# Kernel tuning notes

Hardware: AMD Instinct MI355X
Metric: run time of the kernel (lower is better)

Reference implementation:

```python
import jax, jax.numpy as jnp
import numpy as np

# Matches init_kwargs: zip(dilation_rates, sequence_lengths)
DILATION_RATES = (1, 2, 4)
SEQUENCE_LENGTHS = (2048, 4096, 8192)


def setup_inputs() -> dict:
    key = jax.random.key(0)
    qkv = jax.random.normal(key, (4, 8192, 3, 16, 64), dtype=jnp.float32)
    return {"qkv": qkv}


def _attend(x, scale):
    # x: (B', Nseg, 3, h, d) -- vanilla softmax attention over axis Nseg
    q, k, v = x[:, :, 0], x[:, :, 1], x[:, :, 2]
    scores = jnp.einsum('bnhd,bmhd->bhnm', q, k) * scale
    attn = jax.nn.softmax(scores, axis=-1)
    return jnp.einsum('bhnm,bmhd->bnhd', attn, v)  # (B', Nseg, h, d)


def reference(qkv):
    b, n, _, h, d = qkv.shape
    scale = 1.0 / jnp.sqrt(jnp.asarray(d, qkv.dtype))  # softmax_scale=None default
    out = jnp.zeros((b, n, h, d), qkv.dtype)
    for r, s in zip(DILATION_RATES, SEQUENCE_LENGTHS):
        nseg = n // s
        # 'b (n s) qkv h d -> b n s qkv h d' then dilated slice [::r]
        x = qkv.reshape(b, nseg, s, 3, h, d)[:, :, ::r]  # (b, nseg, sp, 3, h, d)
        sp = x.shape[2]
        # 'b n s qkv h d -> (b s) n qkv h d'
        x = x.transpose(0, 2, 1, 3, 4, 5).reshape(b * sp, nseg, 3, h, d)
        o = _attend(x, scale)  # (b*sp, nseg, h, d)
        # '(b s) n h d -> b n s h d'
        o = o.reshape(b, sp, nseg, h, d).transpose(0, 2, 1, 3, 4)
        # strided scatter-add back into the full-length accumulator
        out = out.reshape(b, nseg, s, h, d).at[:, :, ::r].add(o).reshape(b, n, h, d)
    # final global normalization over the sequence dim (as in the source)
    return out / out.sum(axis=1, keepdims=True)
```

## Files before the change

### kernel.cpp

```cpp
#include <hip/hip_runtime.h>

constexpr int   Bn    = 4;
constexpr int   Nn    = 8192;
constexpr int   Hn    = 16;
constexpr int   Dn    = 64;
constexpr int   ROW   = 3 * Hn * Dn;
constexpr long long QKV_B = (long long)Nn * ROW;
constexpr int   OUT_N = Hn * Dn;
constexpr long long OUT_B = (long long)Nn * OUT_N;

template<int CTRL>
__device__ __forceinline__ float dpp_add(float x) {
  int mv = __builtin_amdgcn_update_dpp(0, __float_as_int(x), CTRL, 0xF, 0xF, true);
  return x + __int_as_float(mv);
}
__device__ __forceinline__ float row16_sum(float x) {
  x = dpp_add<0xB1>(x);
  x = dpp_add<0x4E>(x);
  x = dpp_add<0x124>(x);
  x = dpp_add<0x128>(x);
  return x;
}

__global__ __launch_bounds__(256) void dil_main(const float* __restrict__ qkv,
                                                float* __restrict__ out,
                                                double* __restrict__ colsum,
                                                int repMask) {
  __shared__ float lds[4][2048];
  const int tid  = threadIdx.x;
  const int h    = tid >> 4;
  const int t16  = tid & 15;
  const int bid  = blockIdx.x;
  const int b    = bid >> 9;
  const int jbase= bid & 511;

  const float* qb = qkv + (size_t)b * QKV_B;
  float*       ob = out + (size_t)b * OUT_B;

  float cs[4] = {0.f, 0.f, 0.f, 0.f};

  for (int it = 0; it < 4; ++it) {
    const int j = jbase + it * 512;
    if (it) __syncthreads();

#pragma unroll
    for (int c = 0; c < 8; ++c) {
      const int f   = c * 1024 + tid * 4;
      const int m   = f >> 11;
      const int off = f & 2047;
      const float4 t = *(const float4*)(qb + (size_t)(m * 2048 + j) * ROW + off);
      *(float4*)(&lds[m][off]) = t;
    }

    float v[4][4];
#pragma unroll
    for (int m = 0; m < 4; ++m) {
      const float4 t = *(const float4*)(qb + (size_t)(m * 2048 + j) * ROW +
                                        2048 + h * 64 + t16 * 4);
      v[m][0] = t.x; v[m][1] = t.y; v[m][2] = t.z; v[m][3] = t.w;
    }

    __syncthreads();

    float q[4][4], k[4][4];
#pragma unroll
    for (int m = 0; m < 4; ++m) {
      float4 t = *(const float4*)(&lds[m][h * 64 + t16 * 4]);
      q[m][0] = t.x; q[m][1] = t.y; q[m][2] = t.z; q[m][3] = t.w;
      t = *(const float4*)(&lds[m][1024 + h * 64 + t16 * 4]);
      k[m][0] = t.x; k[m][1] = t.y; k[m][2] = t.z; k[m][3] = t.w;
    }

    float S[4][4];
#pragma unroll
    for (int m = 0; m < 4; ++m)
#pragma unroll
      for (int m2 = 0; m2 < 4; ++m2) {
        float s = q[m][0] * k[m2][0] + q[m][1] * k[m2][1] +
                  q[m][2] * k[m2][2] + q[m][3] * k[m2][3];
        S[m][m2] = row16_sum(s) * 0.125f;
      }

    float acc[4][4];

#pragma unroll
    for (int m = 0; m < 4; ++m) {
      float mx = fmaxf(fmaxf(S[m][0], S[m][1]), fmaxf(S[m][2], S[m][3]));
      float e0 = __expf(S[m][0] - mx);
      float e1 = __expf(S[m][1] - mx);
      float e2 = __expf(S[m][2] - mx);
      float e3 = __expf(S[m][3] - mx);
      float inv = 1.0f / (e0 + e1 + e2 + e3);
      e0 *= inv; e1 *= inv; e2 *= inv; e3 *= inv;
#pragma unroll
      for (int c = 0; c < 4; ++c)
        acc[m][c] = e0 * v[0][c] + e1 * v[1][c] + e2 * v[2][c] + e3 * v[3][c];
    }

    if ((j & 1) == 0) {
#pragma unroll
      for (int m = 0; m < 4; ++m) {
        const int a  = m & 1;
        const int b2 = a + 2;
        float sa = S[m][a], sb = S[m][b2];
        float mx = fmaxf(sa, sb);
        float ea = __expf(sa - mx);
        float eb = __expf(sb - mx);
        float inv = 1.0f / (ea + eb);
        ea *= inv; eb *= inv;
#pragma unroll
        for (int c = 0; c < 4; ++c)
          acc[m][c] += ea * v[a][c] + eb * v[b2][c];
      }
    }

    if ((j & 3) == 0) {
#pragma unroll
      for (int m = 0; m < 4; ++m)
#pragma unroll
        for (int c = 0; c < 4; ++c)
          acc[m][c] += v[m][c];
    }

#pragma unroll
    for (int m = 0; m < 4; ++m) {
      float4 st = make_float4(acc[m][0], acc[m][1], acc[m][2], acc[m][3]);
      *(float4*)(ob + (size_t)(m * 2048 + j) * OUT_N + h * 64 + t16 * 4) = st;
      cs[0] += acc[m][0]; cs[1] += acc[m][1];
      cs[2] += acc[m][2]; cs[3] += acc[m][3];
    }
  }

  double* cp = colsum + (size_t)(bid & repMask) * 4096 +
               ((size_t)b * 16 + h) * 64 + t16 * 4;
  atomicAdd(cp + 0, (double)cs[0]);
  atomicAdd(cp + 1, (double)cs[1]);
  atomicAdd(cp + 2, (double)cs[2]);
  atomicAdd(cp + 3, (double)cs[3]);
}

__global__ __launch_bounds__(256) void dil_recip(const double* __restrict__ colsum,
                                                 float* __restrict__ recip, int rep) {
  const int i = blockIdx.x * 256 + threadIdx.x;
  if (i < Bn * Hn * Dn) {
    double s = 0.0;
    for (int r = 0; r < rep; ++r) s += colsum[(size_t)r * 4096 + i];
    recip[i] = (float)(1.0 / s);
  }
}

__global__ __launch_bounds__(256) void dil_scale(float* __restrict__ out,
                                                 const float* __restrict__ recip) {
  const long long f = (long long)blockIdx.x * 256 + threadIdx.x;
  const int d4 = (int)(f & 15);
  const int h  = (int)((f >> 4) & 15);
  const int b  = (int)(f >> 21);
  const float4 r = ((const float4*)recip)[(b * 16 + h) * 16 + d4];
  float4 o = ((const float4*)out)[f];
  o.x *= r.x; o.y *= r.y; o.z *= r.z; o.w *= r.w;
  ((float4*)out)[f] = o;
}

extern "C" void kernel_launch(void* const* d_in, const int* in_sizes, int n_in,
                              void* d_out, int out_size, void* d_ws, size_t ws_size,
                              hipStream_t stream) {
  const float* qkv = (const float*)d_in[0];
  float* out = (float*)d_out;

  int rep = 32;
  while (rep > 1 &&
         (size_t)rep * 4096 * sizeof(double) + 4096 * sizeof(float) > ws_size)
    rep >>= 1;

  double* colsum = (double*)d_ws;
  float*  recip  = (float*)((char*)d_ws + (size_t)rep * 4096 * sizeof(double));

  hipMemsetAsync(d_ws, 0, (size_t)rep * 4096 * sizeof(double), stream);

  dil_main<<<2048, 256, 0, stream>>>(qkv, out, colsum, rep - 1);

  dil_recip<<<16, 256, 0, stream>>>(colsum, recip, rep);

  const long long nf4 = (long long)Bn * Nn * Hn * Dn / 4;
  dil_scale<<<(int)(nf4 / 256), 256, 0, stream>>>(out, recip);
}
```

Baseline: 179.0 us.

## Store unnormalized output as bf16 in workspace and drop LDS staging

The main kernel now writes the unnormalized accumulator as bf16 into a workspace buffer. The scale kernel reads those bf16 values and writes the normalized fp32 output, which cuts intermediate write and read traffic roughly in half. Q, K and V are also loaded straight from global memory into registers, replacing the LDS staging and its barriers. The bf16 intermediate loses precision before normalization and could break accuracy tolerances, and it needs a large workspace; if the workspace is too small the code falls back to the fp32 path.

New measurement: 179.8 us. About the same (+0.5%).

```diff
diff --git a/kernel.cpp b/kernel.cpp
--- a/kernel.cpp
+++ b/kernel.cpp
@@ -8,6 +8,7 @@
 constexpr long long QKV_B = (long long)Nn * ROW;
 constexpr int   OUT_N = Hn * Dn;
 constexpr long long OUT_B = (long long)Nn * OUT_N;
+constexpr long long OUT_TOT = (long long)Bn * OUT_B;
 
 template<int CTRL>
 __device__ __forceinline__ float dpp_add(float x) {
@@ -22,11 +23,18 @@
   return x;
 }
 
+__device__ __forceinline__ unsigned short f2bf_rne(float x) {
+  unsigned u = __float_as_uint(x);
+  u += 0x7FFFu + ((u >> 16) & 1u);
+  return (unsigned short)(u >> 16);
+}
+
+template<bool USE_BF16>
 __global__ __launch_bounds__(256) void dil_main(const float* __restrict__ qkv,
                                                 float* __restrict__ out,
+                                                unsigned short* __restrict__ ws16,
                                                 double* __restrict__ colsum,
                                                 int repMask) {
-  __shared__ float lds[4][2048];
   const int tid  = threadIdx.x;
   const int h    = tid >> 4;
   const int t16  = tid & 15;
@@ -34,41 +42,25 @@
   const int b    = bid >> 9;
   const int jbase= bid & 511;
 
-  const float* qb = qkv + (size_t)b * QKV_B;
-  float*       ob = out + (size_t)b * OUT_B;
+  const float* qb = qkv + (size_t)b * QKV_B + tid * 4;
+  const size_t obase = (size_t)b * OUT_B + tid * 4;
 
   float cs[4] = {0.f, 0.f, 0.f, 0.f};
 
   for (int it = 0; it < 4; ++it) {
     const int j = jbase + it * 512;
-    if (it) __syncthreads();
-
-#pragma unroll
-    for (int c = 0; c < 8; ++c) {
-      const int f   = c * 1024 + tid * 4;
-      const int m   = f >> 11;
-      const int off = f & 2047;
-      const float4 t = *(const float4*)(qb + (size_t)(m * 2048 + j) * ROW + off);
-      *(float4*)(&lds[m][off]) = t;
-    }
-
-    float v[4][4];
+
+    float q[4][4], k[4][4], v[4][4];
 #pragma unroll
     for (int m = 0; m < 4; ++m) {
-      const float4 t = *(const float4*)(qb + (size_t)(m * 2048 + j) * ROW +
-                                        2048 + h * 64 + t16 * 4);
+      const float* rp = qb + (size_t)(m * 2048 + j) * ROW;
+      float4 t;
+      t = *(const float4*)(rp);
+      q[m][0] = t.x; q[m][1] = t.y; q[m][2] = t.z; q[m][3] = t.w;
+      t = *(const float4*)(rp + 1024);
+      k[m][0] = t.x; k[m][1] = t.y; k[m][2] = t.z; k[m][3] = t.w;
+      t = *(const float4*)(rp + 2048);
       v[m][0] = t.x; v[m][1] = t.y; v[m][2] = t.z; v[m][3] = t.w;
-    }
-
-    __syncthreads();
-
-    float q[4][4], k[4][4];
-#pragma unroll
-    for (int m = 0; m < 4; ++m) {
-      float4 t = *(const float4*)(&lds[m][h * 64 + t16 * 4]);
-      q[m][0] = t.x; q[m][1] = t.y; q[m][2] = t.z; q[m][3] = t.w;
-      t = *(const float4*)(&lds[m][1024 + h * 64 + t16 * 4]);
-      k[m][0] = t.x; k[m][1] = t.y; k[m][2] = t.z; k[m][3] = t.w;
     }
 
     float S[4][4];
@@ -124,8 +116,16 @@
 
 #pragma unroll
     for (int m = 0; m < 4; ++m) {
-      float4 st = make_float4(acc[m][0], acc[m][1], acc[m][2], acc[m][3]);
-      *(float4*)(ob + (size_t)(m * 2048 + j) * OUT_N + h * 64 + t16 * 4) = st;
+      const size_t oi = obase + (size_t)(m * 2048 + j) * OUT_N;
+      if (USE_BF16) {
+        ushort4 st;
+        st.x = f2bf_rne(acc[m][0]); st.y = f2bf_rne(acc[m][1]);
+        st.z = f2bf_rne(acc[m][2]); st.w = f2bf_rne(acc[m][3]);
+        *(ushort4*)(ws16 + oi) = st;
+      } else {
+        *(float4*)(out + oi) =
+            make_float4(acc[m][0], acc[m][1], acc[m][2], acc[m][3]);
+      }
       cs[0] += acc[m][0]; cs[1] += acc[m][1];
       cs[2] += acc[m][2]; cs[3] += acc[m][3];
     }
@@ -149,8 +149,34 @@
   }
 }
 
-__global__ __launch_bounds__(256) void dil_scale(float* __restrict__ out,
-                                                 const float* __restrict__ recip) {
+__global__ __launch_bounds__(256) void dil_scale_bf16(const unsigned short* __restrict__ ws16,
+                                                      float* __restrict__ out,
+                                                      const float* __restrict__ recip) {
+  const long long u = (long long)blockIdx.x * 256 + threadIdx.x;
+  const long long e = u * 8;
+  const int b  = (int)(e >> 23);
+  const int h  = (int)((e >> 6) & 15);
+  const int q8 = (int)((e >> 3) & 7);
+
+  const float4 r0 = ((const float4*)recip)[((b * 16 + h) << 4) + q8 * 2];
+  const float4 r1 = ((const float4*)recip)[((b * 16 + h) << 4) + q8 * 2 + 1];
+
+  const uint4 raw = *(const uint4*)(ws16 + e);
+  float4 o0, o1;
+  o0.x = __uint_as_float((raw.x & 0xFFFFu) << 16) * r0.x;
+  o0.y = __uint_as_float((raw.x & 0xFFFF0000u))   * r0.y;
+  o0.z = __uint_as_float((raw.y & 0xFFFFu) << 16) * r0.z;
+  o0.w = __uint_as_float((raw.y & 0xFFFF0000u))   * r0.w;
+  o1.x = __uint_as_float((raw.z & 0xFFFFu) << 16) * r1.x;
+  o1.y = __uint_as_float((raw.z & 0xFFFF0000u))   * r1.y;
+  o1.z = __uint_as_float((raw.w & 0xFFFFu) << 16) * r1.z;
+  o1.w = __uint_as_float((raw.w & 0xFFFF0000u))   * r1.w;
+  *(float4*)(out + e)     = o0;
+  *(float4*)(out + e + 4) = o1;
+}
+
+__global__ __launch_bounds__(256) void dil_scale_f32(float* __restrict__ out,
+                                                     const float* __restrict__ recip) {
   const long long f = (long long)blockIdx.x * 256 + threadIdx.x;
   const int d4 = (int)(f & 15);
   const int h  = (int)((f >> 4) & 15);
@@ -167,20 +193,40 @@
   const float* qkv = (const float*)d_in[0];
   float* out = (float*)d_out;
 
+  const size_t bf16_bytes = (size_t)OUT_TOT * 2;
   int rep = 32;
-  while (rep > 1 &&
-         (size_t)rep * 4096 * sizeof(double) + 4096 * sizeof(float) > ws_size)
+  bool use_bf16 = true;
+  while (rep > 1 && bf16_bytes + (size_t)rep * 4096 * sizeof(double) +
+                        4096 * sizeof(float) > ws_size)
     rep >>= 1;
-
-  double* colsum = (double*)d_ws;
-  float*  recip  = (float*)((char*)d_ws + (size_t)rep * 4096 * sizeof(double));
-
-  hipMemsetAsync(d_ws, 0, (size_t)rep * 4096 * sizeof(double), stream);
-
-  dil_main<<<2048, 256, 0, stream>>>(qkv, out, colsum, rep - 1);
+  if (bf16_bytes + (size_t)rep * 4096 * sizeof(double) + 4096 * sizeof(float) >
+      ws_size) {
+    use_bf16 = false;
+    rep = 32;
+    while (rep > 1 && (size_t)rep * 4096 * sizeof(double) +
+                          4096 * sizeof(float) > ws_size)
+      rep >>= 1;
+  }
+
+  unsigned short* ws16 = (unsigned short*)d_ws;
+  char* tail = (char*)d_ws + (use_bf16 ? bf16_bytes : 0);
+  double* colsum = (double*)tail;
+  float*  recip  = (float*)(tail + (size_t)rep * 4096 * sizeof(double));
+
+  hipMemsetAsync(colsum, 0, (size_t)rep * 4096 * sizeof(double), stream);
+
+  if (use_bf16)
+    dil_main<true><<<2048, 256, 0, stream>>>(qkv, out, ws16, colsum, rep - 1);
+  else
+    dil_main<false><<<2048, 256, 0, stream>>>(qkv, out, ws16, colsum, rep - 1);
 
   dil_recip<<<16, 256, 0, stream>>>(colsum, recip, rep);
 
-  const long long nf4 = (long long)Bn * Nn * Hn * Dn / 4;
-  dil_scale<<<(int)(nf4 / 256), 256, 0, stream>>>(out, recip);
-}
+  if (use_bf16) {
+    const long long nu = OUT_TOT / 8;
+    dil_scale_bf16<<<(int)(nu / 256), 256, 0, stream>>>(ws16, out, recip);
+  } else {
+    const long long nf4 = OUT_TOT / 4;
+    dil_scale_f32<<<(int)(nf4 / 256), 256, 0, stream>>>(out, recip);
+  }
+}
```
